# Performance work log

Hardware: AMD Instinct MI355X
Metric: run time of the kernel (lower is better)

The kernel has to match this reference:

```python
import jax, jax.numpy as jnp
import numpy as np

B, S, D = 32, 8192, 64


def setup_inputs() -> dict:
    key = jax.random.key(0)
    k1, k2 = jax.random.split(key)
    input_real = jax.random.normal(k1, (B, S, D), dtype=jnp.float32)
    input_imag = jax.random.normal(k2, (B, S, D), dtype=jnp.float32)
    return {"input_real": input_real, "input_imag": input_imag}


def reference(input_real, input_imag):
    # ComplexMixture: mean over seq of per-token complex outer products v v^H.
    # Original builds [B,S,D,D] via 4 batch_dots then means over S; fused here
    # as Gram contractions over the sequence axis (no [B,S,D,D] intermediate).
    seq_len = input_real.shape[1]
    inv_s = jnp.asarray(1.0 / seq_len, dtype=input_real.dtype)
    rr = jnp.einsum('bsi,bsj->bij', input_real, input_real)
    ii = jnp.einsum('bsi,bsj->bij', input_imag, input_imag)
    ri = jnp.einsum('bsi,bsj->bij', input_real, input_imag)
    out_real = (rr + ii) * inv_s                     # [B, D, D], symmetric
    out_imag = (ri - jnp.swapaxes(ri, 1, 2)) * inv_s  # [B, D, D], antisymmetric
    return (out_real, out_imag)
```

## Files before the change

### kernel.cpp

```cpp
#include <hip/hip_runtime.h>


#define BATCH 32
#define SEQ   8192
#define DD    64
#define BK    64

typedef __bf16 bf16x8 __attribute__((ext_vector_type(8)));
typedef float  f32x16 __attribute__((ext_vector_type(16)));

#define GLD_LDS16(gp, lp) \
  __builtin_amdgcn_global_load_lds( \
      (const __attribute__((address_space(1))) void*)(gp), \
      (__attribute__((address_space(3))) void*)(lp), 16, 0, 0)

__device__ __forceinline__ unsigned bf16pk(float a, float b) {
  unsigned ua = __builtin_bit_cast(unsigned, a);
  unsigned ub = __builtin_bit_cast(unsigned, b);
  ua = (ua + 0x7fffu + ((ua >> 16) & 1u)) >> 16;
  ub = (ub + 0x7fffu + ((ub >> 16) & 1u)) >> 16;
  return (ua & 0xffffu) | (ub << 16);
}

__device__ __forceinline__ bf16x8 ldsfrag(const float* p) {
  float f0 = p[0*64], f1 = p[1*64], f2 = p[2*64], f3 = p[3*64];
  float f4 = p[4*64], f5 = p[5*64], f6 = p[6*64], f7 = p[7*64];
  uint4 q;
  q.x = bf16pk(f0, f1); q.y = bf16pk(f2, f3);
  q.z = bf16pk(f4, f5); q.w = bf16pk(f6, f7);
  return __builtin_bit_cast(bf16x8, q);
}

#define MFMA(a, b, c) __builtin_amdgcn_mfma_f32_32x32x16_bf16((a), (b), (c), 0, 0, 0)

template<int CHUNKS>
__global__ __launch_bounds__(256, 4) void gram_partial(
    const float* __restrict__ R, const float* __restrict__ I,
    float* __restrict__ ws)
{
  constexpr int SCHUNK = SEQ / CHUNKS;
  constexpr int NIT    = SCHUNK / BK;
  __shared__ float lds[8320];
  float* ldsR = lds;
  float* ldsI = lds + 4096;

  const int tid  = threadIdx.x;
  const int wave = tid >> 6;
  const int lane = tid & 63;
  const int l31  = lane & 31;
  const int lhi  = lane >> 5;
  const int b = blockIdx.x & 31;
  const int c = blockIdx.x >> 5;
  const float* Rb = R + (size_t)b * (SEQ * DD);
  const float* Ib = I + (size_t)b * (SEQ * DD);

  f32x16 acc0 = {};
  f32x16 acc1 = {};

  const int chunk0 = c * SCHUNK;

  for (int it = 0; it < NIT; ++it) {
    const float* gR = Rb + (size_t)(chunk0 + it * BK) * DD;
    const float* gI = Ib + (size_t)(chunk0 + it * BK) * DD;
    #pragma unroll
    for (int t = 0; t < 4; ++t) {
      const int row0 = wave * 16 + t * 4;
      GLD_LDS16(gR + row0 * 64 + lane * 4, &ldsR[row0 * 64]);
      GLD_LDS16(gI + row0 * 64 + lane * 4, &ldsI[row0 * 64]);
    }
    __syncthreads();
    #pragma unroll
    for (int ks = 0; ks < 4; ++ks) {
      const int kb = (ks * 16 + lhi * 8) * 64 + l31;
      const float* pR = &ldsR[kb];
      const float* pI = &ldsI[kb];
      if (wave == 0) {
        bf16x8 r0 = ldsfrag(pR), i0 = ldsfrag(pI);
        acc0 = MFMA(r0, r0, acc0);
        acc0 = MFMA(i0, i0, acc0);
        acc1 = MFMA(r0, i0, acc1);
      } else if (wave == 1) {
        bf16x8 r0 = ldsfrag(pR), r32 = ldsfrag(pR + 32);
        bf16x8 i0 = ldsfrag(pI), i32 = ldsfrag(pI + 32);
        acc0 = MFMA(r0, r32, acc0);
        acc0 = MFMA(i0, i32, acc0);
      } else if (wave == 2) {
        bf16x8 r0 = ldsfrag(pR), r32 = ldsfrag(pR + 32);
        bf16x8 i0 = ldsfrag(pI), i32 = ldsfrag(pI + 32);
        acc0 = MFMA(r32, i0, acc0);
        acc1 = MFMA(r0, i32, acc1);
      } else {
        bf16x8 r32 = ldsfrag(pR + 32), i32 = ldsfrag(pI + 32);
        acc0 = MFMA(r32, r32, acc0);
        acc0 = MFMA(i32, i32, acc0);
        acc1 = MFMA(r32, i32, acc1);
      }
    }
    __syncthreads();
  }

  float* ldsS = lds;
  float* ldsM = lds + 4160;
  const int jj = l31;
  #pragma unroll
  for (int r = 0; r < 16; ++r) {
    const int ii = (r & 3) + 8 * (r >> 2) + 4 * lhi;
    if (wave == 0) {
      ldsS[ii * 65 + jj]               = acc0[r];
      ldsM[ii * 65 + jj]               = acc1[r];
    } else if (wave == 1) {
      ldsS[ii * 65 + 32 + jj]          = acc0[r];
    } else if (wave == 2) {
      ldsM[(32 + ii) * 65 + jj]        = acc0[r];
      ldsM[ii * 65 + 32 + jj]          = acc1[r];
    } else {
      ldsS[(32 + ii) * 65 + 32 + jj]   = acc0[r];
      ldsM[(32 + ii) * 65 + 32 + jj]   = acc1[r];
    }
  }
  __syncthreads();
  float* wsS = ws + ((size_t)(c * 32 + b) * 2) * 4096;
  float* wsM = wsS + 4096;
  #pragma unroll
  for (int k = 0; k < 16; ++k) {
    const int e = tid + 256 * k;
    const int i = e >> 6, j = e & 63;
    const float sv = (i >= 32 && j < 32) ? ldsS[j * 65 + i] : ldsS[i * 65 + j];
    wsS[e] = sv;
    wsM[e] = ldsM[i * 65 + j] - ldsM[j * 65 + i];
  }
}

template<int CHUNKS>
__global__ __launch_bounds__(256) void gram_reduce(
    const float4* __restrict__ ws, float4* __restrict__ out)
{
  const int o = blockIdx.x * 256 + threadIdx.x;
  const int kind = o >> 15;
  const int rem  = o & 32767;
  const int b    = rem >> 10;
  const int e    = rem & 1023;
  const float inv = 1.0f / (float)SEQ;
  float sx = 0.f, sy = 0.f, sz = 0.f, sw = 0.f;
  #pragma unroll
  for (int c = 0; c < CHUNKS; ++c) {
    float4 v = ws[((size_t)(c * 32 + b) * 2 + kind) * 1024 + e];
    sx += v.x; sy += v.y; sz += v.z; sw += v.w;
  }
  float4 r; r.x = sx * inv; r.y = sy * inv; r.z = sz * inv; r.w = sw * inv;
  out[o] = r;
}

extern "C" void kernel_launch(void* const* d_in, const int* in_sizes, int n_in,
                              void* d_out, int out_size, void* d_ws, size_t ws_size,
                              hipStream_t stream) {
  const float* R = (const float*)d_in[0];
  const float* I = (const float*)d_in[1];
  float* out = (float*)d_out;
  float* ws  = (float*)d_ws;

  const size_t need32 = (size_t)32 * 32 * 2 * 4096 * 4;
  if (ws_size >= need32) {
    gram_partial<32><<<BATCH * 32, 256, 0, stream>>>(R, I, ws);
    gram_reduce<32><<<256, 256, 0, stream>>>((const float4*)ws, (float4*)out);
  } else {
    gram_partial<16><<<BATCH * 16, 256, 0, stream>>>(R, I, ws);
    gram_reduce<16><<<256, 256, 0, stream>>>((const float4*)ws, (float4*)out);
  }
}
```

Before: 171.9 us.

## Load MFMA fragments directly from global into registers with double buffering

```diff
diff --git a/kernel.cpp b/kernel.cpp
--- a/kernel.cpp
+++ b/kernel.cpp
@@ -4,15 +4,9 @@
 #define BATCH 32
 #define SEQ   8192
 #define DD    64
-#define BK    64
 
 typedef __bf16 bf16x8 __attribute__((ext_vector_type(8)));
 typedef float  f32x16 __attribute__((ext_vector_type(16)));
-
-#define GLD_LDS16(gp, lp) \
-  __builtin_amdgcn_global_load_lds( \
-      (const __attribute__((address_space(1))) void*)(gp), \
-      (__attribute__((address_space(3))) void*)(lp), 16, 0, 0)
 
 __device__ __forceinline__ unsigned bf16pk(float a, float b) {
   unsigned ua = __builtin_bit_cast(unsigned, a);
@@ -22,12 +16,10 @@
   return (ua & 0xffffu) | (ub << 16);
 }
 
-__device__ __forceinline__ bf16x8 ldsfrag(const float* p) {
-  float f0 = p[0*64], f1 = p[1*64], f2 = p[2*64], f3 = p[3*64];
-  float f4 = p[4*64], f5 = p[5*64], f6 = p[6*64], f7 = p[7*64];
+__device__ __forceinline__ bf16x8 pack8(const float* f) {
   uint4 q;
-  q.x = bf16pk(f0, f1); q.y = bf16pk(f2, f3);
-  q.z = bf16pk(f4, f5); q.w = bf16pk(f6, f7);
+  q.x = bf16pk(f[0], f[1]); q.y = bf16pk(f[2], f[3]);
+  q.z = bf16pk(f[4], f[5]); q.w = bf16pk(f[6], f[7]);
   return __builtin_bit_cast(bf16x8, q);
 }
 
@@ -39,10 +31,8 @@
     float* __restrict__ ws)
 {
   constexpr int SCHUNK = SEQ / CHUNKS;
-  constexpr int NIT    = SCHUNK / BK;
-  __shared__ float lds[8320];
-  float* ldsR = lds;
-  float* ldsI = lds + 4096;
+  constexpr int NSTEP  = SCHUNK / 16;
+  __shared__ float lds[2 * 64 * 65];
 
   const int tid  = threadIdx.x;
   const int wave = tid >> 6;
@@ -51,52 +41,60 @@
   const int lhi  = lane >> 5;
   const int b = blockIdx.x & 31;
   const int c = blockIdx.x >> 5;
-  const float* Rb = R + (size_t)b * (SEQ * DD);
-  const float* Ib = I + (size_t)b * (SEQ * DD);
 
-  f32x16 acc0 = {};
-  f32x16 acc1 = {};
+  const bool nR0  = (wave <= 1);
+  const bool nR32 = (wave >= 1);
+  const bool nI0  = (wave <= 2);
+  const bool nI32 = (wave >= 1);
 
-  const int chunk0 = c * SCHUNK;
+  const size_t base0 = (size_t)b * (SEQ * DD) + (size_t)(c * SCHUNK + lhi * 8) * DD + l31;
+  const float* pR = R + base0;
+  const float* pI = I + base0;
 
-  for (int it = 0; it < NIT; ++it) {
-    const float* gR = Rb + (size_t)(chunk0 + it * BK) * DD;
-    const float* gI = Ib + (size_t)(chunk0 + it * BK) * DD;
+  f32x16 acc0 = {}, acc1 = {};
+  float cur[4][8], nxt[4][8];
+
+  auto LOADSTEP = [&](float (&dst)[4][8], int ks) {
+    const float* r = pR + (size_t)ks * (16 * DD);
+    const float* i = pI + (size_t)ks * (16 * DD);
     #pragma unroll
-    for (int t = 0; t < 4; ++t) {
-      const int row0 = wave * 16 + t * 4;
-      GLD_LDS16(gR + row0 * 64 + lane * 4, &ldsR[row0 * 64]);
-      GLD_LDS16(gI + row0 * 64 + lane * 4, &ldsI[row0 * 64]);
+    for (int j = 0; j < 8; ++j) {
+      if (nR0)  dst[0][j] = r[j * DD];
+      if (nR32) dst[1][j] = r[j * DD + 32];
+      if (nI0)  dst[2][j] = i[j * DD];
+      if (nI32) dst[3][j] = i[j * DD + 32];
     }
-    __syncthreads();
-    #pragma unroll
-    for (int ks = 0; ks < 4; ++ks) {
-      const int kb = (ks * 16 + lhi * 8) * 64 + l31;
-      const float* pR = &ldsR[kb];
-      const float* pI = &ldsI[kb];
-      if (wave == 0) {
-        bf16x8 r0 = ldsfrag(pR), i0 = ldsfrag(pI);
-        acc0 = MFMA(r0, r0, acc0);
-        acc0 = MFMA(i0, i0, acc0);
-        acc1 = MFMA(r0, i0, acc1);
-      } else if (wave == 1) {
-        bf16x8 r0 = ldsfrag(pR), r32 = ldsfrag(pR + 32);
-        bf16x8 i0 = ldsfrag(pI), i32 = ldsfrag(pI + 32);
-        acc0 = MFMA(r0, r32, acc0);
-        acc0 = MFMA(i0, i32, acc0);
-      } else if (wave == 2) {
-        bf16x8 r0 = ldsfrag(pR), r32 = ldsfrag(pR + 32);
-        bf16x8 i0 = ldsfrag(pI), i32 = ldsfrag(pI + 32);
-        acc0 = MFMA(r32, i0, acc0);
-        acc1 = MFMA(r0, i32, acc1);
-      } else {
-        bf16x8 r32 = ldsfrag(pR + 32), i32 = ldsfrag(pI + 32);
-        acc0 = MFMA(r32, r32, acc0);
-        acc0 = MFMA(i32, i32, acc0);
-        acc1 = MFMA(r32, i32, acc1);
-      }
+  };
+
+  auto COMPUTE = [&](float (&fr)[4][8]) {
+    if (wave == 0) {
+      bf16x8 r0 = pack8(fr[0]), i0 = pack8(fr[2]);
+      acc0 = MFMA(r0, r0, acc0);
+      acc0 = MFMA(i0, i0, acc0);
+      acc1 = MFMA(r0, i0, acc1);
+    } else if (wave == 1) {
+      bf16x8 r0 = pack8(fr[0]), r32 = pack8(fr[1]);
+      bf16x8 i0 = pack8(fr[2]), i32 = pack8(fr[3]);
+      acc0 = MFMA(r0, r32, acc0);
+      acc0 = MFMA(i0, i32, acc0);
+      acc1 = MFMA(r0, i32, acc1);
+    } else if (wave == 2) {
+      bf16x8 r32 = pack8(fr[1]), i0 = pack8(fr[2]), i32 = pack8(fr[3]);
+      acc0 = MFMA(r32, i0, acc0);
+      acc1 = MFMA(r32, i32, acc1);
+    } else {
+      bf16x8 r32 = pack8(fr[1]), i32 = pack8(fr[3]);
+      acc0 = MFMA(r32, r32, acc0);
+      acc0 = MFMA(i32, i32, acc0);
     }
-    __syncthreads();
+  };
+
+  LOADSTEP(cur, 0);
+  for (int ks = 0; ks < NSTEP; ks += 2) {
+    LOADSTEP(nxt, ks + 1);
+    COMPUTE(cur);
+    if (ks + 2 < NSTEP) LOADSTEP(cur, ks + 2);
+    COMPUTE(nxt);
   }
 
   float* ldsS = lds;
@@ -106,16 +104,16 @@
   for (int r = 0; r < 16; ++r) {
     const int ii = (r & 3) + 8 * (r >> 2) + 4 * lhi;
     if (wave == 0) {
-      ldsS[ii * 65 + jj]               = acc0[r];
-      ldsM[ii * 65 + jj]               = acc1[r];
+      ldsS[ii * 65 + jj]              = acc0[r];
+      ldsM[ii * 65 + jj]              = acc1[r];
     } else if (wave == 1) {
-      ldsS[ii * 65 + 32 + jj]          = acc0[r];
+      ldsS[ii * 65 + 32 + jj]         = acc0[r];
+      ldsM[ii * 65 + 32 + jj]         = acc1[r];
     } else if (wave == 2) {
-      ldsM[(32 + ii) * 65 + jj]        = acc0[r];
-      ldsM[ii * 65 + 32 + jj]          = acc1[r];
+      ldsM[(32 + ii) * 65 + jj]       = acc0[r];
+      ldsM[(32 + ii) * 65 + 32 + jj]  = acc1[r];
     } else {
-      ldsS[(32 + ii) * 65 + 32 + jj]   = acc0[r];
-      ldsM[(32 + ii) * 65 + 32 + jj]   = acc1[r];
+      ldsS[(32 + ii) * 65 + 32 + jj]  = acc0[r];
     }
   }
   __syncthreads();
```

Result: faster. 168.3 us (-2.1%).

## Give each wave its own sequence slice with double-buffered async loads

Applied to the files above, without the earlier changes.

```diff
diff --git a/kernel.cpp b/kernel.cpp
--- a/kernel.cpp
+++ b/kernel.cpp
@@ -1,10 +1,12 @@
 #include <hip/hip_runtime.h>
 
 
-#define BATCH 32
-#define SEQ   8192
-#define DD    64
-#define BK    64
+#define BATCH  32
+#define SEQ    8192
+#define DD     64
+#define CHUNKS 16
+#define SCHUNK (SEQ / CHUNKS)
+#define ROUNDS (SCHUNK / 64)
 
 typedef __bf16 bf16x8 __attribute__((ext_vector_type(8)));
 typedef float  f32x16 __attribute__((ext_vector_type(16)));
@@ -33,17 +35,11 @@
 
 #define MFMA(a, b, c) __builtin_amdgcn_mfma_f32_32x32x16_bf16((a), (b), (c), 0, 0, 0)
 
-template<int CHUNKS>
-__global__ __launch_bounds__(256, 4) void gram_partial(
+__global__ __launch_bounds__(256, 2) void gram_partial(
     const float* __restrict__ R, const float* __restrict__ I,
     float* __restrict__ ws)
 {
-  constexpr int SCHUNK = SEQ / CHUNKS;
-  constexpr int NIT    = SCHUNK / BK;
-  __shared__ float lds[8320];
-  float* ldsR = lds;
-  float* ldsI = lds + 4096;
-
+  __shared__ float lds[16384];
   const int tid  = threadIdx.x;
   const int wave = tid >> 6;
   const int lane = tid & 63;
@@ -51,87 +47,84 @@
   const int lhi  = lane >> 5;
   const int b = blockIdx.x & 31;
   const int c = blockIdx.x >> 5;
-  const float* Rb = R + (size_t)b * (SEQ * DD);
-  const float* Ib = I + (size_t)b * (SEQ * DD);
 
-  f32x16 acc0 = {};
-  f32x16 acc1 = {};
+  float* myb = lds + wave * 4096;
+  const size_t g0 = (size_t)b * (SEQ * DD) + (size_t)(c * SCHUNK + wave * 16) * DD;
+  const float* gR = R + g0;
+  const float* gI = I + g0;
 
-  const int chunk0 = c * SCHUNK;
+  f32x16 aS0 = {}, aS1 = {}, aS2 = {};
+  f32x16 aM0 = {}, aM1 = {}, aM2 = {}, aM3 = {};
 
-  for (int it = 0; it < NIT; ++it) {
-    const float* gR = Rb + (size_t)(chunk0 + it * BK) * DD;
-    const float* gI = Ib + (size_t)(chunk0 + it * BK) * DD;
+  auto ISSUE = [&](int rnd, int p) {
+    const float* r = gR + (size_t)rnd * (64 * DD);
+    const float* i = gI + (size_t)rnd * (64 * DD);
+    float* d = myb + p * 2048;
     #pragma unroll
     for (int t = 0; t < 4; ++t) {
-      const int row0 = wave * 16 + t * 4;
-      GLD_LDS16(gR + row0 * 64 + lane * 4, &ldsR[row0 * 64]);
-      GLD_LDS16(gI + row0 * 64 + lane * 4, &ldsI[row0 * 64]);
+      GLD_LDS16(r + t * 256 + lane * 4, d + t * 256);
+      GLD_LDS16(i + t * 256 + lane * 4, d + 1024 + t * 256);
     }
-    __syncthreads();
-    #pragma unroll
-    for (int ks = 0; ks < 4; ++ks) {
-      const int kb = (ks * 16 + lhi * 8) * 64 + l31;
-      const float* pR = &ldsR[kb];
-      const float* pI = &ldsI[kb];
-      if (wave == 0) {
-        bf16x8 r0 = ldsfrag(pR), i0 = ldsfrag(pI);
-        acc0 = MFMA(r0, r0, acc0);
-        acc0 = MFMA(i0, i0, acc0);
-        acc1 = MFMA(r0, i0, acc1);
-      } else if (wave == 1) {
-        bf16x8 r0 = ldsfrag(pR), r32 = ldsfrag(pR + 32);
-        bf16x8 i0 = ldsfrag(pI), i32 = ldsfrag(pI + 32);
-        acc0 = MFMA(r0, r32, acc0);
-        acc0 = MFMA(i0, i32, acc0);
-      } else if (wave == 2) {
-        bf16x8 r0 = ldsfrag(pR), r32 = ldsfrag(pR + 32);
-        bf16x8 i0 = ldsfrag(pI), i32 = ldsfrag(pI + 32);
-        acc0 = MFMA(r32, i0, acc0);
-        acc1 = MFMA(r0, i32, acc1);
-      } else {
-        bf16x8 r32 = ldsfrag(pR + 32), i32 = ldsfrag(pI + 32);
-        acc0 = MFMA(r32, r32, acc0);
-        acc0 = MFMA(i32, i32, acc0);
-        acc1 = MFMA(r32, i32, acc1);
+  };
+
+  ISSUE(0, 0);
+  #pragma unroll
+  for (int r = 0; r < ROUNDS; ++r) {
+    const int p = r & 1;
+    if (r + 1 < ROUNDS) {
+      ISSUE(r + 1, p ^ 1);
+      asm volatile("s_waitcnt vmcnt(8)" ::: "memory");
+    } else {
+      asm volatile("s_waitcnt vmcnt(0)" ::: "memory");
+    }
+    const float* pR = myb + p * 2048 + (lhi * 8) * 64 + l31;
+    const float* pI = pR + 1024;
+    bf16x8 r0  = ldsfrag(pR),      r32 = ldsfrag(pR + 32);
+    bf16x8 i0  = ldsfrag(pI),      i32 = ldsfrag(pI + 32);
+    aS0 = MFMA(r0,  r0,  aS0);  aS0 = MFMA(i0,  i0,  aS0);
+    aS1 = MFMA(r0,  r32, aS1);  aS1 = MFMA(i0,  i32, aS1);
+    aS2 = MFMA(r32, r32, aS2);  aS2 = MFMA(i32, i32, aS2);
+    aM0 = MFMA(r0,  i0,  aM0);
+    aM1 = MFMA(r0,  i32, aM1);
+    aM2 = MFMA(r32, i0,  aM2);
+    aM3 = MFMA(r32, i32, aM3);
+  }
+
+  __syncthreads();
+  float* Sp = lds;
+  float* Mp = lds + 4160;
+  for (int e = tid; e < 8320; e += 256) lds[e] = 0.0f;
+  __syncthreads();
+  #pragma unroll 1
+  for (int w = 0; w < 4; ++w) {
+    if (wave == w) {
+      #pragma unroll
+      for (int r = 0; r < 16; ++r) {
+        const int ii = (r & 3) + 8 * (r >> 2) + 4 * lhi;
+        const int jj = l31;
+        Sp[ii * 65 + jj]              += aS0[r];
+        Sp[ii * 65 + 32 + jj]         += aS1[r];
+        Sp[(32 + ii) * 65 + 32 + jj]  += aS2[r];
+        Mp[ii * 65 + jj]              += aM0[r];
+        Mp[ii * 65 + 32 + jj]         += aM1[r];
+        Mp[(32 + ii) * 65 + jj]       += aM2[r];
+        Mp[(32 + ii) * 65 + 32 + jj]  += aM3[r];
       }
     }
     __syncthreads();
   }
-
-  float* ldsS = lds;
-  float* ldsM = lds + 4160;
-  const int jj = l31;
-  #pragma unroll
-  for (int r = 0; r < 16; ++r) {
-    const int ii = (r & 3) + 8 * (r >> 2) + 4 * lhi;
-    if (wave == 0) {
-      ldsS[ii * 65 + jj]               = acc0[r];
-      ldsM[ii * 65 + jj]               = acc1[r];
-    } else if (wave == 1) {
-      ldsS[ii * 65 + 32 + jj]          = acc0[r];
-    } else if (wave == 2) {
-      ldsM[(32 + ii) * 65 + jj]        = acc0[r];
-      ldsM[ii * 65 + 32 + jj]          = acc1[r];
-    } else {
-      ldsS[(32 + ii) * 65 + 32 + jj]   = acc0[r];
-      ldsM[(32 + ii) * 65 + 32 + jj]   = acc1[r];
-    }
-  }
-  __syncthreads();
   float* wsS = ws + ((size_t)(c * 32 + b) * 2) * 4096;
   float* wsM = wsS + 4096;
   #pragma unroll
   for (int k = 0; k < 16; ++k) {
     const int e = tid + 256 * k;
     const int i = e >> 6, j = e & 63;
-    const float sv = (i >= 32 && j < 32) ? ldsS[j * 65 + i] : ldsS[i * 65 + j];
+    const float sv = (i >= 32 && j < 32) ? Sp[j * 65 + i] : Sp[i * 65 + j];
     wsS[e] = sv;
-    wsM[e] = ldsM[i * 65 + j] - ldsM[j * 65 + i];
+    wsM[e] = Mp[i * 65 + j] - Mp[j * 65 + i];
   }
 }
 
-template<int CHUNKS>
 __global__ __launch_bounds__(256) void gram_reduce(
     const float4* __restrict__ ws, float4* __restrict__ out)
 {
@@ -159,12 +152,6 @@
   float* out = (float*)d_out;
   float* ws  = (float*)d_ws;
 
-  const size_t need32 = (size_t)32 * 32 * 2 * 4096 * 4;
-  if (ws_size >= need32) {
-    gram_partial<32><<<BATCH * 32, 256, 0, stream>>>(R, I, ws);
-    gram_reduce<32><<<256, 256, 0, stream>>>((const float4*)ws, (float4*)out);
-  } else {
-    gram_partial<16><<<BATCH * 16, 256, 0, stream>>>(R, I, ws);
-    gram_reduce<16><<<256, 256, 0, stream>>>((const float4*)ws, (float4*)out);
-  }
+  gram_partial<<<BATCH * CHUNKS, 256, 0, stream>>>(R, I, ws);
+  gram_reduce<<<256, 256, 0, stream>>>((const float4*)ws, (float4*)out);
 }
```

After: 165.8 us. -3.5%, faster.
